# Performance work log

Measured on AMD Instinct MI355X. Metric: run time of the kernel, lower is better.

Reference implementation:

```python
import jax, jax.numpy as jnp
import numpy as np

B, T, C = 1, 2048, 1024
H, HKV, DH, WIN = 16, 4, 64, 128
EPS = 1e-5


def rotate_half(x):
    x1, x2 = jnp.split(x, 2, axis=-1)
    return jnp.concatenate((-x2, x1), axis=-1)


def setup_inputs() -> dict:
    key = jax.random.key(0)
    ks = jax.random.split(key, 8)
    s = 0.02
    return {
        "x": jax.random.normal(ks[0], (B, T, C), dtype=jnp.float32),
        "Wq": jax.random.normal(ks[1], (C, H * DH), dtype=jnp.float32) * s,
        "Wk": jax.random.normal(ks[2], (C, HKV * DH), dtype=jnp.float32) * s,
        "Wv": jax.random.normal(ks[3], (C, HKV * DH), dtype=jnp.float32) * s,
        "Wc": jax.random.normal(ks[4], (C, C), dtype=jnp.float32) * s,
        "Wg": jax.random.normal(ks[5], (C, H), dtype=jnp.float32) * s,
        "bg": jax.random.normal(ks[6], (H,), dtype=jnp.float32) * s,
        "rms_w": jnp.ones((C,), dtype=jnp.float32),
    }


def reference(x, Wq, Wk, Wv, Wc, Wg, bg, rms_w):
    n_rep = H // HKV
    # projections -> [B, heads, T, DH]
    q = (x @ Wq).reshape(B, T, H, DH).transpose(0, 2, 1, 3)
    k = (x @ Wk).reshape(B, T, HKV, DH).transpose(0, 2, 1, 3)
    v = (x @ Wv).reshape(B, T, HKV, DH).transpose(0, 2, 1, 3)
    # rotary embedding (freqs duplicated across the two halves)
    inv_freq = 1.0 / (10000.0 ** (jnp.arange(0, DH, 2, dtype=jnp.float32) / DH))
    freqs = jnp.arange(T, dtype=jnp.float32)[:, None] * inv_freq[None, :]
    emb = jnp.concatenate((freqs, freqs), axis=-1)  # [T, DH]
    cos, sin = jnp.cos(emb)[None, None], jnp.sin(emb)[None, None]
    q = q * cos + rotate_half(q) * sin
    k = k * cos + rotate_half(k) * sin
    # GQA: repeat kv heads (contiguous repeat matches torch expand+reshape)
    k = jnp.repeat(k, n_rep, axis=1)
    v = jnp.repeat(v, n_rep, axis=1)
    # gated decay
    gate_logits = (x @ Wg + bg).reshape(B, T, H, 1).transpose(0, 2, 1, 3)  # [B,H,T,1]
    log_alpha = jax.nn.log_sigmoid(gate_logits)
    log_in_scale = jax.nn.log_sigmoid(-gate_logits)
    k_scaled = k * jnp.exp(log_in_scale)
    la_cum = jnp.cumsum(log_alpha, axis=2)                  # [B,H,T,1]
    log_decay = la_cum - jnp.swapaxes(la_cum, 2, 3)         # [B,H,T,T]
    causal = jnp.triu(jnp.ones((T, T), dtype=bool), k=1)
    decay = jnp.exp(jnp.where(causal, -jnp.inf, log_decay))
    scores = jnp.einsum('bhtd,bhsd->bhts', q, k_scaled)
    y_global = jnp.einsum('bhts,bhsd->bhtd', scores * decay, v)
    nb = T // WIN
    qb = q.reshape(B, H, nb, WIN, DH)
    kb = k.reshape(B, H, nb, WIN, DH)
    vb = v.reshape(B, H, nb, WIN, DH)
    att = jnp.einsum('bhnqd,bhnkd->bhnqk', qb, kb) / jnp.sqrt(jnp.float32(DH))
    wmask = jnp.triu(jnp.ones((WIN, WIN), dtype=bool), k=1)
    att = jax.nn.softmax(jnp.where(wmask, -jnp.inf, att), axis=-1)
    y_local = jnp.einsum('bhnqk,bhnkd->bhnqd', att, vb).reshape(B, H, T, DH)
    # fuse, RMSNorm, output projection
    y = (y_global + y_local).transpose(0, 2, 1, 3).reshape(B, T, C)
    y = y * jax.lax.rsqrt(jnp.mean(y * y, axis=-1, keepdims=True) + EPS) * rms_w
    return y @ Wc
```

## Files before the change

kernel.cpp:

```cpp
#include <hip/hip_runtime.h>
#include <hip/hip_bf16.h>


typedef __attribute__((ext_vector_type(8))) short bf16x8;
typedef __attribute__((ext_vector_type(4))) float f32x4;

#define MFMA16(a, b, c) __builtin_amdgcn_mfma_f32_16x16x32_bf16(a, b, c, 0, 0, 0)
#define LN10000_OVER_32 0.28782313662425575f

__device__ __forceinline__ short f2b(float f) {
  __hip_bfloat16 h = __float2bfloat16(f);
  return *reinterpret_cast<short*>(&h);
}
__device__ __forceinline__ float b2f(short s) {
  return __uint_as_float(((unsigned)(unsigned short)s) << 16);
}
__device__ __forceinline__ void gload16(const void* g, void* l) {
  __builtin_amdgcn_global_load_lds(
      (const __attribute__((address_space(1))) void*)g,
      (__attribute__((address_space(3))) void*)l, 16, 0, 0);
}

__device__ __forceinline__ void transpose_cvt_body(
    const float* __restrict__ src, short* __restrict__ dst, int R, int C,
    int bx, int by, float* ts ) {
  int c0 = bx * 32, r0 = by * 32;
  int tr = threadIdx.x >> 3, tc = (threadIdx.x & 7) * 4;
  float4 v = *(const float4*)&src[(size_t)(r0 + tr) * C + c0 + tc];
  ts[tr * 33 + tc] = v.x;
  ts[tr * 33 + tc + 1] = v.y;
  ts[tr * 33 + tc + 2] = v.z;
  ts[tr * 33 + tc + 3] = v.w;
  __syncthreads();
  alignas(8) short o[4];
#pragma unroll
  for (int i = 0; i < 4; ++i) o[i] = f2b(ts[(tc + i) * 33 + tr]);
  *(uint2*)&dst[(size_t)(c0 + tr) * R + r0 + tc] = *(uint2*)o;
}

__global__ __launch_bounds__(256) void prep_fused(
    const float* __restrict__ x, const float* __restrict__ Wq,
    const float* __restrict__ Wk, const float* __restrict__ Wv,
    const float* __restrict__ Wc, const float* __restrict__ Wg,
    const float* __restrict__ bg, short* __restrict__ xb,
    short* __restrict__ wqkvT, short* __restrict__ wcT,
    float* __restrict__ g) {
  __shared__ float ts[32 * 33];
  const int j = blockIdx.x;
  const int tid = threadIdx.x;
  if (j < 2048) {
    const int t = j;
    const int h = tid & 15, chunk = tid >> 4;
    const float* xr = x + (size_t)t * 1024 + chunk * 64;
    const float* wg = Wg + (size_t)chunk * 64 * 16 + h;
    float acc = 0.f;
#pragma unroll
    for (int c = 0; c < 64; c += 4) {
      float4 xv = *(const float4*)(xr + c);
      acc = fmaf(xv.x, wg[(c + 0) * 16], acc);
      acc = fmaf(xv.y, wg[(c + 1) * 16], acc);
      acc = fmaf(xv.z, wg[(c + 2) * 16], acc);
      acc = fmaf(xv.w, wg[(c + 3) * 16], acc);
    }
    ts[chunk * 16 + h] = acc;
    __syncthreads();
    if (tid < 16) {
      float s = bg[tid];
#pragma unroll
      for (int i = 0; i < 16; ++i) s += ts[i * 16 + tid];
      g[t * 16 + tid] = s;
    }
  } else if (j < 3072) {
    int i = ((j - 2048) * 256 + tid) * 8;
    float4 a = *(const float4*)(x + i);
    float4 b = *(const float4*)(x + i + 4);
    alignas(16) short o[8] = {f2b(a.x), f2b(a.y), f2b(a.z), f2b(a.w),
                              f2b(b.x), f2b(b.y), f2b(b.z), f2b(b.w)};
    *(float4*)(xb + i) = *(float4*)o;
  } else if (j < 4096) {
    int jj = j - 3072;
    transpose_cvt_body(Wq, wqkvT, 1024, 1024, jj & 31, jj >> 5, ts);
  } else if (j < 4352) {
    int jj = j - 4096;
    transpose_cvt_body(Wk, wqkvT + 1024 * 1024, 1024, 256, jj & 7, jj >> 3, ts);
  } else if (j < 4608) {
    int jj = j - 4352;
    transpose_cvt_body(Wv, wqkvT + 1280 * 1024, 1024, 256, jj & 7, jj >> 3, ts);
  } else {
    int jj = j - 4608;
    transpose_cvt_body(Wc, wcT, 1024, 1024, jj & 31, jj >> 5, ts);
  }
}

__global__ __launch_bounds__(256) void qkv_gemm_fused(
    const short* __restrict__ A, const short* __restrict__ Bt,
    short* __restrict__ qkvb, short* __restrict__ vtb,
    short* __restrict__ ktb, const float* __restrict__ g,
    float* __restrict__ lac, float* __restrict__ insc) {
  __shared__ short As[64 * 64];
  __shared__ short Bs[64 * 64];
  __shared__ float part[256];
  const int id = blockIdx.x;
  const int tid = threadIdx.x;
  if (id >= 768) {
    const int h = id - 768;
    float vals[8];
    float local = 0.f;
#pragma unroll
    for (int i = 0; i < 8; ++i) {
      int t = tid * 8 + i;
      float gv = g[t * 16 + h];
      float la = (gv > 0.f) ? -log1pf(expf(-gv)) : (gv - log1pf(expf(gv)));
      insc[h * 2048 + t] = 1.f / (1.f + expf(gv));
      vals[i] = la;
      local += la;
    }
    part[tid] = local;
    __syncthreads();
    for (int off = 1; off < 256; off <<= 1) {
      float add = (tid >= off) ? part[tid - off] : 0.f;
      __syncthreads();
      part[tid] += add;
      __syncthreads();
    }
    float run = (tid > 0) ? part[tid - 1] : 0.f;
#pragma unroll
    for (int i = 0; i < 8; ++i) {
      run += vals[i];
      lac[h * 2048 + tid * 8 + i] = run;
    }
    return;
  }
  const int lane = tid & 63, wid = tid >> 6;
  const int l15 = lane & 15, lq = lane >> 4;
  const int jlin = id >> 3;
  const int by = (id & 7) + 8 * (jlin / 24);
  const int bx = jlin % 24;
  const int m0 = by * 64, n0 = bx * 64;
  const int K = 1024;
  const int srow = lane >> 3;
  const int sc16 = (lane & 7) ^ srow;
  f32x4 acc[4];
#pragma unroll
  for (int nt = 0; nt < 4; ++nt) acc[nt] = {0.f, 0.f, 0.f, 0.f};
  for (int kt = 0; kt < K; kt += 64) {
    __syncthreads();
#pragma unroll
    for (int i = 0; i < 2; ++i) {
      int jj = wid * 2 + i;
      int row = jj * 8 + srow;
      gload16(A + (size_t)(m0 + row) * K + kt + sc16 * 8, &As[jj * 512]);
      gload16(Bt + (size_t)(n0 + row) * K + kt + sc16 * 8, &Bs[jj * 512]);
    }
    __syncthreads();
    bf16x8 af[2], bfr[4][2];
#pragma unroll
    for (int ks = 0; ks < 2; ++ks) {
      int c16 = ks * 4 + lq;
      int ar = wid * 16 + l15;
      af[ks] = *(const bf16x8*)&As[(ar * 8 + (c16 ^ (ar & 7))) * 8];
#pragma unroll
      for (int nt = 0; nt < 4; ++nt) {
        int br = nt * 16 + l15;
        bfr[nt][ks] = *(const bf16x8*)&Bs[(br * 8 + (c16 ^ (br & 7))) * 8];
      }
    }
#pragma unroll
    for (int ks = 0; ks < 2; ++ks)
#pragma unroll
      for (int nt = 0; nt < 4; ++nt)
        acc[nt] = MFMA16(af[ks], bfr[nt][ks], acc[nt]);
  }
  const int row0 = m0 + wid * 16 + lq * 4;
  if (bx >= 20) {
#pragma unroll
    for (int nt = 0; nt < 4; ++nt) {
      int vcol = (n0 - 1280) + nt * 16 + l15;
      alignas(8) short o4[4];
#pragma unroll
      for (int r = 0; r < 4; ++r) o4[r] = f2b(acc[nt][r]);
      *(uint2*)&vtb[(size_t)vcol * 2048 + row0] = *(uint2*)o4;
    }
    return;
  }
  const bool isk = (bx >= 16);
#pragma unroll
  for (int nt = 0; nt < 2; ++nt) {
    int d = nt * 16 + l15;
    float ivf = __expf(-LN10000_OVER_32 * (float)d);
    alignas(8) short oa[4], ob[4];
#pragma unroll
    for (int r = 0; r < 4; ++r) {
      int row_g = row0 + r;
      float th = (float)row_g * ivf;
      float cs = cosf(th), sn = sinf(th);
      float a = acc[nt][r], b = acc[nt + 2][r];
      oa[r] = f2b(a * cs - b * sn);
      ob[r] = f2b(b * cs + a * sn);
      qkvb[(size_t)row_g * 1536 + n0 + d] = oa[r];
      qkvb[(size_t)row_g * 1536 + n0 + d + 32] = ob[r];
    }
    if (isk) {
      int dk = n0 - 1024 + d;
      *(uint2*)&ktb[(size_t)dk * 2048 + row0] = *(uint2*)oa;
      *(uint2*)&ktb[(size_t)(dk + 32) * 2048 + row0] = *(uint2*)ob;
    }
  }
}

__global__ __launch_bounds__(256) void p1_local(
    const short* __restrict__ qkv, const short* __restrict__ vtb,
    const short* __restrict__ ktb, const float* __restrict__ lac,
    const float* __restrict__ insc, float* __restrict__ Bmat,
    short* __restrict__ yl) {
  __shared__ short SA[64 * 64];
  __shared__ short SB[128 * 64];
  __shared__ short SC[64 * 128];
  __shared__ short SD[64 * 128];
  __shared__ float lacs[64], inss[64], gvals[64];
  const int tid = threadIdx.x, lane = tid & 63, wid = tid >> 6;
  const int l15 = lane & 15, lq = lane >> 4;
  const int h = blockIdx.y;
  const int kh = h >> 2;
  if (blockIdx.z == 0) {
    const int c = blockIdx.x;
    short* Ks = SB;
    short* Vts = SC;
    const int srow = lane >> 3;
    const int sc16 = (lane & 7) ^ srow;
#pragma unroll
    for (int i = 0; i < 2; ++i) {
      int jj = wid * 2 + i;
      int row = jj * 8 + srow;
      gload16(ktb + (size_t)(kh * 64 + row) * 2048 + c * 64 + sc16 * 8,
              &Ks[jj * 512]);
      gload16(vtb + (size_t)(kh * 64 + row) * 2048 + c * 64 + sc16 * 8,
              &Vts[jj * 512]);
    }
    if (tid < 64) {
      lacs[tid] = lac[h * 2048 + c * 64 + tid];
      inss[tid] = insc[h * 2048 + c * 64 + tid];
    }
    __syncthreads();
    if (tid < 64)
      gvals[tid] = __expf(fminf(lacs[63] - lacs[tid], 0.f)) * inss[tid];
    __syncthreads();
    const int er = wid * 16 + l15;
    bf16x8 av[2];
#pragma unroll
    for (int ks = 0; ks < 2; ++ks) {
      int c16 = ks * 4 + lq;
      bf16x8 raw = *(const bf16x8*)&Vts[(er * 8 + (c16 ^ (er & 7))) * 8];
      float4 g0 = *(const float4*)&gvals[c16 * 8];
      float4 g1 = *(const float4*)&gvals[c16 * 8 + 4];
      float gv[8] = {g0.x, g0.y, g0.z, g0.w, g1.x, g1.y, g1.z, g1.w};
      bf16x8 sc;
#pragma unroll
      for (int jx = 0; jx < 8; ++jx) sc[jx] = f2b(b2f(raw[jx]) * gv[jx]);
      av[ks] = sc;
    }
    f32x4 acc[4];
#pragma unroll
    for (int nt = 0; nt < 4; ++nt) acc[nt] = {0.f, 0.f, 0.f, 0.f};
#pragma unroll
    for (int ks = 0; ks < 2; ++ks) {
      int c16 = ks * 4 + lq;
#pragma unroll
      for (int nt = 0; nt < 4; ++nt) {
        int dr = nt * 16 + l15;
        bf16x8 bk = *(const bf16x8*)&Ks[(dr * 8 + (c16 ^ (dr & 7))) * 8];
        acc[nt] = MFMA16(av[ks], bk, acc[nt]);
      }
    }
    float* Bout = Bmat + (size_t)(h * 32 + c) * 4096;
#pragma unroll
    for (int nt = 0; nt < 4; ++nt)
#pragma unroll
      for (int r = 0; r < 4; ++r) {
        int e = wid * 16 + lq * 4 + r;
        Bout[e * 64 + nt * 16 + l15] = acc[nt][r];
      }
  } else {
    const int half = blockIdx.x & 1, wb = blockIdx.x >> 1;
    const int t0 = wb * 128;
    short* Qs = SA;
    short* Ks = SB;
    short* Vts = SC;
    short* Ps = SD;
#pragma unroll
    for (int i = 0; i < 2; ++i) {
      int cix = tid + 256 * i;
      int row = cix >> 3, cc = cix & 7;
      *(float4*)&Qs[(row * 8 + (cc ^ (row & 7))) * 8] =
          *(const float4*)&qkv[(size_t)(t0 + half * 64 + row) * 1536 + h * 64 + cc * 8];
    }
#pragma unroll
    for (int i = 0; i < 4; ++i) {
      int cix = tid + 256 * i;
      int row = cix >> 3, cc = cix & 7;
      *(float4*)&Ks[(row * 8 + (cc ^ (row & 7))) * 8] =
          *(const float4*)&qkv[(size_t)(t0 + row) * 1536 + 1024 + kh * 64 + cc * 8];
    }
#pragma unroll
    for (int i = 0; i < 4; ++i) {
      int cix = tid + 256 * i;
      int row = cix >> 4, cc = cix & 15;
      int sw = (row * 16 + ((cc & 8) | ((cc & 7) ^ (row & 7)))) * 8;
      *(float4*)&Vts[sw] =
          *(const float4*)&vtb[(size_t)(kh * 64 + row) * 2048 + t0 + cc * 8];
    }
    __syncthreads();
    const int qr = wid * 16 + l15;
    bf16x8 aq[2];
#pragma unroll
    for (int ks = 0; ks < 2; ++ks) {
      int c16 = ks * 4 + lq;
      aq[ks] = *(const bf16x8*)&Qs[(qr * 8 + (c16 ^ (qr & 7))) * 8];
    }
    f32x4 sv[2][4];
    const int nst = half + 1;
    for (int st = 0; st < nst; ++st)
#pragma unroll
      for (int nt = 0; nt < 4; ++nt) {
        int kr = st * 64 + nt * 16 + l15;
        bf16x8 bk0 = *(const bf16x8*)&Ks[(kr * 8 + ((0 + lq) ^ (kr & 7))) * 8];
        bf16x8 bk1 = *(const bf16x8*)&Ks[(kr * 8 + ((4 + lq) ^ (kr & 7))) * 8];
        f32x4 z = {0.f, 0.f, 0.f, 0.f};
        z = MFMA16(aq[0], bk0, z);
        z = MFMA16(aq[1], bk1, z);
        sv[st][nt] = z;
      }
    float mrow[4], ssum[4];
#pragma unroll
    for (int r = 0; r < 4; ++r) mrow[r] = -1e30f;
    for (int st = 0; st < nst; ++st)
#pragma unroll
      for (int nt = 0; nt < 4; ++nt) {
        int col = st * 64 + nt * 16 + l15;
#pragma unroll
        for (int r = 0; r < 4; ++r) {
          int row = half * 64 + wid * 16 + lq * 4 + r;
          float v = (col <= row) ? sv[st][nt][r] * 0.125f : -1e30f;
          sv[st][nt][r] = v;
          mrow[r] = fmaxf(mrow[r], v);
        }
      }
#pragma unroll
    for (int r = 0; r < 4; ++r) {
      for (int off = 1; off < 16; off <<= 1)
        mrow[r] = fmaxf(mrow[r], __shfl_xor(mrow[r], off, 64));
      ssum[r] = 0.f;
    }
    for (int st = 0; st < nst; ++st)
#pragma unroll
      for (int nt = 0; nt < 4; ++nt) {
        int col = st * 64 + nt * 16 + l15;
#pragma unroll
        for (int r = 0; r < 4; ++r) {
          float e = __expf(sv[st][nt][r] - mrow[r]);
          ssum[r] += e;
          int row = wid * 16 + lq * 4 + r;
          int c16 = col >> 3;
          Ps[(row * 16 + ((c16 & 8) | ((c16 & 7) ^ (row & 7)))) * 8 + (col & 7)] =
              f2b(e);
        }
      }
#pragma unroll
    for (int r = 0; r < 4; ++r) {
      for (int off = 1; off < 16; off <<= 1) ssum[r] += __shfl_xor(ssum[r], off, 64);
      ssum[r] = 1.f / ssum[r];
    }
    __syncthreads();
    f32x4 o[4];
#pragma unroll
    for (int nt = 0; nt < 4; ++nt) o[nt] = {0.f, 0.f, 0.f, 0.f};
    for (int ks = 0; ks < nst * 2; ++ks) {
      int c16 = ks * 4 + lq;
      bf16x8 ap = *(const bf16x8*)&Ps[(qr * 16 + ((c16 & 8) | ((c16 & 7) ^ (qr & 7)))) * 8];
#pragma unroll
      for (int nt = 0; nt < 4; ++nt) {
        int vr = nt * 16 + l15;
        bf16x8 bv = *(const bf16x8*)&Vts[(vr * 16 + ((c16 & 8) | ((c16 & 7) ^ (vr & 7)))) * 8];
        o[nt] = MFMA16(ap, bv, o[nt]);
      }
    }
#pragma unroll
    for (int nt = 0; nt < 4; ++nt)
#pragma unroll
      for (int r = 0; r < 4; ++r) {
        int row_g = t0 + half * 64 + wid * 16 + lq * 4 + r;
        int colg = h * 64 + nt * 16 + l15;
        yl[(size_t)row_g * 1024 + colg] = f2b(o[nt][r] * ssum[r]);
      }
  }
}

__global__ __launch_bounds__(256) void global_attn_v3(
    const short* __restrict__ qkv, const short* __restrict__ vtb,
    const float* __restrict__ Bmat, const float* __restrict__ lac,
    const float* __restrict__ insc, short* __restrict__ yg) {
  const int c = blockIdx.x, h = blockIdx.y;
  const int kh = h >> 2;
  __shared__ short Qs[64 * 64], Ks[64 * 64], Vts[64 * 64], Sts[64 * 64],
      Ps[64 * 64];
  __shared__ float lacq[64], inss[64], lacE[32];
  const int tid = threadIdx.x, lane = tid & 63, wid = tid >> 6;
  const int l15 = lane & 15, lq = lane >> 4;
  const int srow = lane >> 3;
  const int sc16 = (lane & 7) ^ srow;
#pragma unroll
  for (int i = 0; i < 2; ++i) {
    int jj = wid * 2 + i;
    int row = jj * 8 + srow;
    gload16(qkv + (size_t)(c * 64 + row) * 1536 + h * 64 + sc16 * 8,
            &Qs[jj * 512]);
    gload16(qkv + (size_t)(c * 64 + row) * 1536 + 1024 + kh * 64 + sc16 * 8,
            &Ks[jj * 512]);
    gload16(vtb + (size_t)(kh * 64 + row) * 2048 + c * 64 + sc16 * 8,
            &Vts[jj * 512]);
  }
  if (tid < 64) {
    lacq[tid] = lac[h * 2048 + c * 64 + tid];
    inss[tid] = insc[h * 2048 + c * 64 + tid];
  }
  if (tid >= 64 && tid < 96) lacE[tid - 64] = lac[h * 2048 + (tid - 64) * 64 + 63];
  __syncthreads();
  const int e = tid >> 2, d0 = (tid & 3) * 16;
  const float laE = (c > 0) ? lacE[c - 1] : 0.f;
  float S[16];
#pragma unroll
  for (int i = 0; i < 16; ++i) S[i] = 0.f;
  for (int cp = 0; cp < c; ++cp) {
    float wgt = __expf(fminf(laE - lacE[cp], 0.f));
    const float* Bp = Bmat + (size_t)(h * 32 + cp) * 4096 + e * 64 + d0;
    float4 b0 = *(const float4*)(Bp + 0);
    float4 b1 = *(const float4*)(Bp + 4);
    float4 b2 = *(const float4*)(Bp + 8);
    float4 b3 = *(const float4*)(Bp + 12);
    S[0] = fmaf(wgt, b0.x, S[0]);  S[1] = fmaf(wgt, b0.y, S[1]);
    S[2] = fmaf(wgt, b0.z, S[2]);  S[3] = fmaf(wgt, b0.w, S[3]);
    S[4] = fmaf(wgt, b1.x, S[4]);  S[5] = fmaf(wgt, b1.y, S[5]);
    S[6] = fmaf(wgt, b1.z, S[6]);  S[7] = fmaf(wgt, b1.w, S[7]);
    S[8] = fmaf(wgt, b2.x, S[8]);  S[9] = fmaf(wgt, b2.y, S[9]);
    S[10] = fmaf(wgt, b2.z, S[10]); S[11] = fmaf(wgt, b2.w, S[11]);
    S[12] = fmaf(wgt, b3.x, S[12]); S[13] = fmaf(wgt, b3.y, S[13]);
    S[14] = fmaf(wgt, b3.z, S[14]); S[15] = fmaf(wgt, b3.w, S[15]);
  }
  {
    alignas(16) short s8[8];
#pragma unroll
    for (int half = 0; half < 2; ++half) {
      int c16 = (tid & 3) * 2 + half;
#pragma unroll
      for (int i = 0; i < 8; ++i) s8[i] = f2b(S[half * 8 + i]);
      *(uint4*)&Sts[(e * 8 + (c16 ^ (e & 7))) * 8] = *(uint4*)s8;
    }
  }
  const int qr = wid * 16 + l15;
  bf16x8 aq[2];
#pragma unroll
  for (int ks = 0; ks < 2; ++ks) {
    int c16 = ks * 4 + lq;
    aq[ks] = *(const bf16x8*)&Qs[(qr * 8 + (c16 ^ (qr & 7))) * 8];
  }
  f32x4 sv[4];
#pragma unroll
  for (int nt = 0; nt < 4; ++nt) {
    int kr = nt * 16 + l15;
    bf16x8 bk0 = *(const bf16x8*)&Ks[(kr * 8 + ((0 + lq) ^ (kr & 7))) * 8];
    bf16x8 bk1 = *(const bf16x8*)&Ks[(kr * 8 + ((4 + lq) ^ (kr & 7))) * 8];
    f32x4 z = {0.f, 0.f, 0.f, 0.f};
    z = MFMA16(aq[0], bk0, z);
    z = MFMA16(aq[1], bk1, z);
    sv[nt] = z;
  }
#pragma unroll
  for (int nt = 0; nt < 4; ++nt) {
    int col = nt * 16 + l15;
    float ls = lacq[col], is = inss[col];
#pragma unroll
    for (int r = 0; r < 4; ++r) {
      int row = wid * 16 + lq * 4 + r;
      float d = lacq[row] - ls;
      float w = __expf(fminf(d, 0.f)) * is;
      if (col > row) w = 0.f;
      Ps[(row * 8 + ((col >> 3) ^ (row & 7))) * 8 + (col & 7)] = f2b(sv[nt][r] * w);
    }
  }
  __syncthreads();
  f32x4 oi[4];
#pragma unroll
  for (int nt = 0; nt < 4; ++nt) {
    int er = nt * 16 + l15;
    bf16x8 bs0 = *(const bf16x8*)&Sts[(er * 8 + ((0 + lq) ^ (er & 7))) * 8];
    bf16x8 bs1 = *(const bf16x8*)&Sts[(er * 8 + ((4 + lq) ^ (er & 7))) * 8];
    f32x4 z = {0.f, 0.f, 0.f, 0.f};
    z = MFMA16(aq[0], bs0, z);
    z = MFMA16(aq[1], bs1, z);
    oi[nt] = z;
  }
  bf16x8 ap[2];
#pragma unroll
  for (int ks = 0; ks < 2; ++ks) {
    int c16 = ks * 4 + lq;
    ap[ks] = *(const bf16x8*)&Ps[(qr * 8 + (c16 ^ (qr & 7))) * 8];
  }
  f32x4 o[4];
#pragma unroll
  for (int nt = 0; nt < 4; ++nt) {
    int vr = nt * 16 + l15;
    bf16x8 bv0 = *(const bf16x8*)&Vts[(vr * 8 + ((0 + lq) ^ (vr & 7))) * 8];
    bf16x8 bv1 = *(const bf16x8*)&Vts[(vr * 8 + ((4 + lq) ^ (vr & 7))) * 8];
    f32x4 z = {0.f, 0.f, 0.f, 0.f};
    z = MFMA16(ap[0], bv0, z);
    z = MFMA16(ap[1], bv1, z);
    o[nt] = z;
  }
  const float laprev = (c > 0) ? lacE[c - 1] : 1e30f;
#pragma unroll
  for (int r = 0; r < 4; ++r) {
    int row = wid * 16 + lq * 4 + r;
    float rfac = __expf(fminf(lacq[row] - laprev, 0.f));
    int row_g = c * 64 + row;
#pragma unroll
    for (int nt = 0; nt < 4; ++nt) {
      int colg = h * 64 + nt * 16 + l15;
      yg[(size_t)row_g * 1024 + colg] = f2b(o[nt][r] + rfac * oi[nt][r]);
    }
  }
}

__global__ __launch_bounds__(256) void out_gemm_rms(
    const short* __restrict__ yg, const short* __restrict__ ylc,
    const float* __restrict__ w, const short* __restrict__ Bt,
    float* __restrict__ C) {
  __shared__ short As[64 * 64];
  __shared__ short Bs[64 * 64];
  __shared__ float ssq_sh[64 * 4];
  __shared__ float sArr[64];
  const int tid = threadIdx.x, lane = tid & 63, wid = tid >> 6;
  const int l15 = lane & 15, lq = lane >> 4;
  const int id = blockIdx.x;
  const int jlin = id >> 3;
  const int by = (id & 7) + 8 * (jlin / 16);
  const int bx = jlin % 16;
  const int m0 = by * 64, n0 = bx * 64;
  const int srow = lane >> 3;
  const int sc16 = (lane & 7) ^ srow;
  const int arow = tid >> 2, akc = (tid & 3) * 16;
  f32x4 acc[4];
#pragma unroll
  for (int nt = 0; nt < 4; ++nt) acc[nt] = {0.f, 0.f, 0.f, 0.f};
  float ssq = 0.f;
  for (int kt = 0; kt < 1024; kt += 64) {
    __syncthreads();
#pragma unroll
    for (int i = 0; i < 2; ++i) {
      int jj = wid * 2 + i;
      int row = jj * 8 + srow;
      gload16(Bt + (size_t)(n0 + row) * 1024 + kt + sc16 * 8, &Bs[jj * 512]);
    }
    {
      const size_t ab = (size_t)(m0 + arow) * 1024 + kt + akc;
      bf16x8 g0 = *(const bf16x8*)&yg[ab];
      bf16x8 g1 = *(const bf16x8*)&yg[ab + 8];
      bf16x8 L0 = *(const bf16x8*)&ylc[ab];
      bf16x8 L1 = *(const bf16x8*)&ylc[ab + 8];
      float4 w0 = *(const float4*)&w[kt + akc];
      float4 w1 = *(const float4*)&w[kt + akc + 4];
      float4 w2 = *(const float4*)&w[kt + akc + 8];
      float4 w3 = *(const float4*)&w[kt + akc + 12];
      float wv[16] = {w0.x, w0.y, w0.z, w0.w, w1.x, w1.y, w1.z, w1.w,
                      w2.x, w2.y, w2.z, w2.w, w3.x, w3.y, w3.z, w3.w};
      alignas(16) short p0[8], p1[8];
#pragma unroll
      for (int i = 0; i < 8; ++i) {
        float yv = b2f(g0[i]) + b2f(L0[i]);
        ssq = fmaf(yv, yv, ssq);
        p0[i] = f2b(yv * wv[i]);
        float yv2 = b2f(g1[i]) + b2f(L1[i]);
        ssq = fmaf(yv2, yv2, ssq);
        p1[i] = f2b(yv2 * wv[8 + i]);
      }
      int c16a = (tid & 3) * 2;
      *(uint4*)&As[(arow * 8 + (c16a ^ (arow & 7))) * 8] = *(uint4*)p0;
      *(uint4*)&As[(arow * 8 + ((c16a + 1) ^ (arow & 7))) * 8] = *(uint4*)p1;
    }
    __syncthreads();
    bf16x8 af[2], bfr[4][2];
#pragma unroll
    for (int ks = 0; ks < 2; ++ks) {
      int c16 = ks * 4 + lq;
      int ar = wid * 16 + l15;
      af[ks] = *(const bf16x8*)&As[(ar * 8 + (c16 ^ (ar & 7))) * 8];
#pragma unroll
      for (int nt = 0; nt < 4; ++nt) {
        int br = nt * 16 + l15;
        bfr[nt][ks] = *(const bf16x8*)&Bs[(br * 8 + (c16 ^ (br & 7))) * 8];
      }
    }
#pragma unroll
    for (int ks = 0; ks < 2; ++ks)
#pragma unroll
      for (int nt = 0; nt < 4; ++nt)
        acc[nt] = MFMA16(af[ks], bfr[nt][ks], acc[nt]);
  }
  __syncthreads();
  ssq_sh[arow * 4 + (tid & 3)] = ssq;
  __syncthreads();
  if (tid < 64) {
    float s = ssq_sh[tid * 4] + ssq_sh[tid * 4 + 1] + ssq_sh[tid * 4 + 2] +
              ssq_sh[tid * 4 + 3];
    sArr[tid] = rsqrtf(s * (1.0f / 1024.0f) + 1e-5f);
  }
  __syncthreads();
#pragma unroll
  for (int r = 0; r < 4; ++r) {
    int row = wid * 16 + lq * 4 + r;
    float scale = sArr[row];
    int row_g = m0 + row;
#pragma unroll
    for (int nt = 0; nt < 4; ++nt)
      C[(size_t)row_g * 1024 + n0 + nt * 16 + l15] = acc[nt][r] * scale;
  }
}

extern "C" void kernel_launch(void* const* d_in, const int* in_sizes, int n_in,
                              void* d_out, int out_size, void* d_ws,
                              size_t ws_size, hipStream_t stream) {
  const float* x = (const float*)d_in[0];
  const float* Wq = (const float*)d_in[1];
  const float* Wk = (const float*)d_in[2];
  const float* Wv = (const float*)d_in[3];
  const float* Wc = (const float*)d_in[4];
  const float* Wg = (const float*)d_in[5];
  const float* bg = (const float*)d_in[6];
  const float* rmsw = (const float*)d_in[7];
  float* out = (float*)d_out;

  short* wqkvT = (short*)d_ws;
  short* wcT = wqkvT + 1536 * 1024;
  short* qkvb = wcT + 1024 * 1024;
  short* vtb = qkvb + 2048 * 1536;
  short* ktb = vtb + 256 * 2048;
  float* gw = (float*)(ktb + 256 * 2048);
  float* lacw = gw + 2048 * 16;
  float* inscw = lacw + 16 * 2048;
  float* Bmat = inscw + 16 * 2048;
  short* xb = (short*)(Bmat + 16 * 32 * 4096);
  short* yg = xb;
  short* ylc = xb + 2048 * 1024;

  prep_fused<<<5632, 256, 0, stream>>>(x, Wq, Wk, Wv, Wc, Wg, bg, xb, wqkvT,
                                       wcT, gw);
  qkv_gemm_fused<<<784, 256, 0, stream>>>(xb, wqkvT, qkvb, vtb, ktb, gw, lacw,
                                          inscw);
  p1_local<<<dim3(32, 16, 2), 256, 0, stream>>>(qkvb, vtb, ktb, lacw, inscw,
                                                Bmat, ylc);
  global_attn_v3<<<dim3(32, 16), 256, 0, stream>>>(qkvb, vtb, Bmat, lacw,
                                                   inscw, yg);
  out_gemm_rms<<<512, 256, 0, stream>>>(yg, ylc, rmsw, wcT, out);
}
```

Baseline: 149.0 us.

## Fuse five kernel launches into one persistent megakernel with grid barriers

```diff
diff --git a/kernel.cpp b/kernel.cpp
--- a/kernel.cpp
+++ b/kernel.cpp
@@ -7,6 +7,8 @@
 
 #define MFMA16(a, b, c) __builtin_amdgcn_mfma_f32_16x16x32_bf16(a, b, c, 0, 0, 0)
 #define LN10000_OVER_32 0.28782313662425575f
+#define GRID 512
+#define SMEM_BYTES 43008
 
 __device__ __forceinline__ short f2b(float f) {
   __hip_bfloat16 h = __float2bfloat16(f);
@@ -21,9 +23,22 @@
       (__attribute__((address_space(3))) void*)l, 16, 0, 0);
 }
 
+__device__ __forceinline__ void gbar(unsigned* ctr, unsigned tgt) {
+  __syncthreads();
+  if (threadIdx.x == 0) {
+    __threadfence();
+    __hip_atomic_fetch_add(ctr, 1u, __ATOMIC_ACQ_REL, __HIP_MEMORY_SCOPE_AGENT);
+    while (__hip_atomic_load(ctr, __ATOMIC_ACQUIRE, __HIP_MEMORY_SCOPE_AGENT) <
+           tgt)
+      __builtin_amdgcn_s_sleep(4);
+    __threadfence();
+  }
+  __syncthreads();
+}
+
 __device__ __forceinline__ void transpose_cvt_body(
     const float* __restrict__ src, short* __restrict__ dst, int R, int C,
-    int bx, int by, float* ts ) {
+    int bx, int by, float* ts) {
   int c0 = bx * 32, r0 = by * 32;
   int tr = threadIdx.x >> 3, tc = (threadIdx.x & 7) * 4;
   float4 v = *(const float4*)&src[(size_t)(r0 + tr) * C + c0 + tc];
@@ -38,15 +53,11 @@
   *(uint2*)&dst[(size_t)(c0 + tr) * R + r0 + tc] = *(uint2*)o;
 }
 
-__global__ __launch_bounds__(256) void prep_fused(
-    const float* __restrict__ x, const float* __restrict__ Wq,
-    const float* __restrict__ Wk, const float* __restrict__ Wv,
-    const float* __restrict__ Wc, const float* __restrict__ Wg,
-    const float* __restrict__ bg, short* __restrict__ xb,
-    short* __restrict__ wqkvT, short* __restrict__ wcT,
-    float* __restrict__ g) {
-  __shared__ float ts[32 * 33];
-  const int j = blockIdx.x;
+__device__ void p0_unit(int j, char* SMEM, const float* x, const float* Wq,
+                        const float* Wk, const float* Wv, const float* Wc,
+                        const float* Wg, const float* bg, short* xb,
+                        short* wqkvT, short* wcT, float* g) {
+  float* ts = (float*)SMEM;
   const int tid = threadIdx.x;
   if (j < 2048) {
     const int t = j;
@@ -92,15 +103,12 @@
   }
 }
 
-__global__ __launch_bounds__(256) void qkv_gemm_fused(
-    const short* __restrict__ A, const short* __restrict__ Bt,
-    short* __restrict__ qkvb, short* __restrict__ vtb,
-    short* __restrict__ ktb, const float* __restrict__ g,
-    float* __restrict__ lac, float* __restrict__ insc) {
-  __shared__ short As[64 * 64];
-  __shared__ short Bs[64 * 64];
-  __shared__ float part[256];
-  const int id = blockIdx.x;
+__device__ void p1_unit(int id, char* SMEM, const short* A, const short* Bt,
+                        short* qkvb, short* vtb, short* ktb, const float* g,
+                        float* lac, float* insc) {
+  short* As = (short*)SMEM;
+  short* Bs = (short*)(SMEM + 8192);
+  float* part = (float*)(SMEM + 40960);
   const int tid = threadIdx.x;
   if (id >= 768) {
     const int h = id - 768;
@@ -137,20 +145,19 @@
   const int by = (id & 7) + 8 * (jlin / 24);
   const int bx = jlin % 24;
   const int m0 = by * 64, n0 = bx * 64;
-  const int K = 1024;
   const int srow = lane >> 3;
   const int sc16 = (lane & 7) ^ srow;
   f32x4 acc[4];
 #pragma unroll
   for (int nt = 0; nt < 4; ++nt) acc[nt] = {0.f, 0.f, 0.f, 0.f};
-  for (int kt = 0; kt < K; kt += 64) {
+  for (int kt = 0; kt < 1024; kt += 64) {
     __syncthreads();
 #pragma unroll
     for (int i = 0; i < 2; ++i) {
       int jj = wid * 2 + i;
       int row = jj * 8 + srow;
-      gload16(A + (size_t)(m0 + row) * K + kt + sc16 * 8, &As[jj * 512]);
-      gload16(Bt + (size_t)(n0 + row) * K + kt + sc16 * 8, &Bs[jj * 512]);
+      gload16(A + (size_t)(m0 + row) * 1024 + kt + sc16 * 8, &As[jj * 512]);
+      gload16(Bt + (size_t)(n0 + row) * 1024 + kt + sc16 * 8, &Bs[jj * 512]);
     }
     __syncthreads();
     bf16x8 af[2], bfr[4][2];
@@ -208,24 +215,19 @@
   }
 }
 
-__global__ __launch_bounds__(256) void p1_local(
-    const short* __restrict__ qkv, const short* __restrict__ vtb,
-    const short* __restrict__ ktb, const float* __restrict__ lac,
-    const float* __restrict__ insc, float* __restrict__ Bmat,
-    short* __restrict__ yl) {
-  __shared__ short SA[64 * 64];
-  __shared__ short SB[128 * 64];
-  __shared__ short SC[64 * 128];
-  __shared__ short SD[64 * 128];
-  __shared__ float lacs[64], inss[64], gvals[64];
+__device__ void p2_unit(int u, char* SMEM, const short* qkv, const short* vtb,
+                        const short* ktb, const float* lac, const float* insc,
+                        float* Bmat, short* yl) {
   const int tid = threadIdx.x, lane = tid & 63, wid = tid >> 6;
   const int l15 = lane & 15, lq = lane >> 4;
-  const int h = blockIdx.y;
-  const int kh = h >> 2;
-  if (blockIdx.z == 0) {
-    const int c = blockIdx.x;
-    short* Ks = SB;
-    short* Vts = SC;
+  if (u < 512) {
+    const int c = u & 31, h = u >> 5;
+    const int kh = h >> 2;
+    short* Ks = (short*)(SMEM + 8192);
+    short* Vts = (short*)(SMEM + 24576);
+    float* lacs = (float*)(SMEM + 40960);
+    float* inss = (float*)(SMEM + 41216);
+    float* gvals = (float*)(SMEM + 41472);
     const int srow = lane >> 3;
     const int sc16 = (lane & 7) ^ srow;
 #pragma unroll
@@ -281,12 +283,14 @@
         Bout[e * 64 + nt * 16 + l15] = acc[nt][r];
       }
   } else {
-    const int half = blockIdx.x & 1, wb = blockIdx.x >> 1;
-    const int t0 = wb * 128;
-    short* Qs = SA;
-    short* Ks = SB;
-    short* Vts = SC;
-    short* Ps = SD;
+    const int v = u - 512;
+    const int xév = v & 31, h = v >> 5;
+    const int half = xév & 1, wb = xév >> 1;
+    const int kh = h >> 2, t0 = wb * 128;
+    short* Qs = (short*)SMEM;
+    short* Ks = (short*)(SMEM + 8192);
+    short* Vts = (short*)(SMEM + 24576);
+    short* Ps = Ks;
 #pragma unroll
     for (int i = 0; i < 2; ++i) {
       int cix = tid + 256 * i;
@@ -330,6 +334,7 @@
         z = MFMA16(aq[1], bk1, z);
         sv[st][nt] = z;
       }
+    __syncthreads();
     float mrow[4], ssum[4];
 #pragma unroll
     for (int r = 0; r < 4; ++r) mrow[r] = -1e30f;
@@ -340,9 +345,9 @@
 #pragma unroll
         for (int r = 0; r < 4; ++r) {
           int row = half * 64 + wid * 16 + lq * 4 + r;
-          float v = (col <= row) ? sv[st][nt][r] * 0.125f : -1e30f;
-          sv[st][nt][r] = v;
-          mrow[r] = fmaxf(mrow[r], v);
+          float vv = (col <= row) ? sv[st][nt][r] * 0.125f : -1e30f;
+          sv[st][nt][r] = vv;
+          mrow[r] = fmaxf(mrow[r], vv);
         }
       }
 #pragma unroll
@@ -395,15 +400,19 @@
   }
 }
 
-__global__ __launch_bounds__(256) void global_attn_v3(
-    const short* __restrict__ qkv, const short* __restrict__ vtb,
-    const float* __restrict__ Bmat, const float* __restrict__ lac,
-    const float* __restrict__ insc, short* __restrict__ yg) {
-  const int c = blockIdx.x, h = blockIdx.y;
+__device__ void p3_unit(int u, char* SMEM, const short* qkv, const short* vtb,
+                        const float* Bmat, const float* lac, const float* insc,
+                        short* yg) {
+  const int c = u & 31, h = u >> 5;
   const int kh = h >> 2;
-  __shared__ short Qs[64 * 64], Ks[64 * 64], Vts[64 * 64], Sts[64 * 64],
-      Ps[64 * 64];
-  __shared__ float lacq[64], inss[64], lacE[32];
+  short* Qs = (short*)SMEM;
+  short* Ks = (short*)(SMEM + 8192);
+  short* Vts = (short*)(SMEM + 16384);
+  short* Sts = (short*)(SMEM + 24576);
+  short* Ps = (short*)(SMEM + 32768);
+  float* lacq = (float*)(SMEM + 40960);
+  float* inss = (float*)(SMEM + 41216);
+  float* lacE = (float*)(SMEM + 41472);
   const int tid = threadIdx.x, lane = tid & 63, wid = tid >> 6;
   const int l15 = lane & 15, lq = lane >> 4;
   const int srow = lane >> 3;
@@ -437,11 +446,11 @@
     float4 b1 = *(const float4*)(Bp + 4);
     float4 b2 = *(const float4*)(Bp + 8);
     float4 b3 = *(const float4*)(Bp + 12);
-    S[0] = fmaf(wgt, b0.x, S[0]);  S[1] = fmaf(wgt, b0.y, S[1]);
-    S[2] = fmaf(wgt, b0.z, S[2]);  S[3] = fmaf(wgt, b0.w, S[3]);
-    S[4] = fmaf(wgt, b1.x, S[4]);  S[5] = fmaf(wgt, b1.y, S[5]);
-    S[6] = fmaf(wgt, b1.z, S[6]);  S[7] = fmaf(wgt, b1.w, S[7]);
-    S[8] = fmaf(wgt, b2.x, S[8]);  S[9] = fmaf(wgt, b2.y, S[9]);
+    S[0] = fmaf(wgt, b0.x, S[0]);   S[1] = fmaf(wgt, b0.y, S[1]);
+    S[2] = fmaf(wgt, b0.z, S[2]);   S[3] = fmaf(wgt, b0.w, S[3]);
+    S[4] = fmaf(wgt, b1.x, S[4]);   S[5] = fmaf(wgt, b1.y, S[5]);
+    S[6] = fmaf(wgt, b1.z, S[6]);   S[7] = fmaf(wgt, b1.w, S[7]);
+    S[8] = fmaf(wgt, b2.x, S[8]);   S[9] = fmaf(wgt, b2.y, S[9]);
     S[10] = fmaf(wgt, b2.z, S[10]); S[11] = fmaf(wgt, b2.w, S[11]);
     S[12] = fmaf(wgt, b3.x, S[12]); S[13] = fmaf(wgt, b3.y, S[13]);
     S[14] = fmaf(wgt, b3.z, S[14]); S[15] = fmaf(wgt, b3.w, S[15]);
@@ -530,17 +539,14 @@
   }
 }
 
-__global__ __launch_bounds__(256) void out_gemm_rms(
-    const short* __restrict__ yg, const short* __restrict__ ylc,
-    const float* __restrict__ w, const short* __restrict__ Bt,
-    float* __restrict__ C) {
-  __shared__ short As[64 * 64];
-  __shared__ short Bs[64 * 64];
-  __shared__ float ssq_sh[64 * 4];
-  __shared__ float sArr[64];
+__device__ void p4_unit(int id, char* SMEM, const short* yg, const short* ylc,
+                        const float* w, const short* Bt, float* C) {
+  short* As = (short*)SMEM;
+  short* Bs = (short*)(SMEM + 8192);
+  float* ssq_sh = (float*)(SMEM + 40960);
+  float* sArr = (float*)(SMEM + 41984);
   const int tid = threadIdx.x, lane = tid & 63, wid = tid >> 6;
   const int l15 = lane & 15, lq = lane >> 4;
-  const int id = blockIdx.x;
   const int jlin = id >> 3;
   const int by = (id & 7) + 8 * (jlin / 16);
   const int bx = jlin % 16;
@@ -625,6 +631,40 @@
   }
 }
 
+__global__ __launch_bounds__(256, 2) void mega(
+    const float* __restrict__ x, const float* __restrict__ Wq,
+    const float* __restrict__ Wk, const float* __restrict__ Wv,
+    const float* __restrict__ Wc, const float* __restrict__ Wg,
+    const float* __restrict__ bg, const float* __restrict__ rmsw,
+    short* __restrict__ xb, short* __restrict__ wqkvT, short* __restrict__ wcT,
+    float* __restrict__ g, short* __restrict__ qkvb, short* __restrict__ vtb,
+    short* __restrict__ ktb, float* __restrict__ lac,
+    float* __restrict__ insc, float* __restrict__ Bmat,
+    short* __restrict__ yg, short* __restrict__ ylc, float* __restrict__ out,
+    unsigned* __restrict__ ctrs) {
+  __shared__ __align__(16) char SMEM[SMEM_BYTES];
+  const int bid = blockIdx.x;
+  for (int u = bid; u < 5632; u += GRID) {
+    __syncthreads();
+    p0_unit(u, SMEM, x, Wq, Wk, Wv, Wc, Wg, bg, xb, wqkvT, wcT, g);
+    __syncthreads();
+  }
+  gbar(&ctrs[0], GRID);
+  for (int u = bid; u < 784; u += GRID) {
+    __syncthreads();
+    p1_unit(u, SMEM, xb, wqkvT, qkvb, vtb, ktb, g, lac, insc);
+  }
+  gbar(&ctrs[1], GRID);
+  for (int u = bid; u < 1024; u += GRID) {
+    __syncthreads();
+    p2_unit(u, SMEM, qkvb, vtb, ktb, lac, insc, Bmat, ylc);
+  }
+  gbar(&ctrs[2], GRID);
+  p3_unit(bid, SMEM, qkvb, vtb, Bmat, lac, insc, yg);
+  gbar(&ctrs[3], GRID);
+  p4_unit(bid, SMEM, yg, ylc, rmsw, wcT, out);
+}
+
 extern "C" void kernel_launch(void* const* d_in, const int* in_sizes, int n_in,
                               void* d_out, int out_size, void* d_ws,
                               size_t ws_size, hipStream_t stream) {
@@ -650,14 +690,10 @@
   short* xb = (short*)(Bmat + 16 * 32 * 4096);
   short* yg = xb;
   short* ylc = xb + 2048 * 1024;
-
-  prep_fused<<<5632, 256, 0, stream>>>(x, Wq, Wk, Wv, Wc, Wg, bg, xb, wqkvT,
-                                       wcT, gw);
-  qkv_gemm_fused<<<784, 256, 0, stream>>>(xb, wqkvT, qkvb, vtb, ktb, gw, lacw,
-                                          inscw);
-  p1_local<<<dim3(32, 16, 2), 256, 0, stream>>>(qkvb, vtb, ktb, lacw, inscw,
-                                                Bmat, ylc);
-  global_attn_v3<<<dim3(32, 16), 256, 0, stream>>>(qkvb, vtb, Bmat, lacw,
-                                                   inscw, yg);
-  out_gemm_rms<<<512, 256, 0, stream>>>(yg, ylc, rmsw, wcT, out);
-}
+  unsigned* ctrs = (unsigned*)(ylc + 2048 * 1024);
+
+  hipMemsetAsync(ctrs, 0, 32, stream);
+  mega<<<GRID, 256, 0, stream>>>(x, Wq, Wk, Wv, Wc, Wg, bg, rmsw, xb, wqkvT,
+                                 wcT, gw, qkvb, vtb, ktb, lacw, inscw, Bmat,
+                                 yg, ylc, out, ctrs);
+}
```

Result: slower. 566.6 us (+280.4%).
